# Kernel optimization log

Measured on AMD Instinct MI355X. Metric: run time of the kernel, lower is better.

The kernel has to match this reference:

```python
import jax, jax.numpy as jnp
import numpy as np

N = 100_000      # nodes
E = 3_200_000    # edges (avg degree 32)
H = 16           # hidden channels
C_IN, C_OUT = 1, 2


def setup_inputs() -> dict:
    key = jax.random.key(0)
    k1, k2, k3, k4, k5 = jax.random.split(key, 5)
    x = jax.random.normal(k1, (N, C_IN), dtype=jnp.float32)
    src = jax.random.randint(k2, (E,), 0, N, dtype=jnp.int32)
    dst = jax.random.randint(k3, (E,), 0, N, dtype=jnp.int32)
    edge_index = jnp.stack([src, dst])  # [2, E], PyG layout
    # Glorot-style init for the two linear transforms
    W1 = jax.random.normal(k4, (C_IN, H), dtype=jnp.float32) * np.sqrt(2.0 / (C_IN + H))
    b1 = jnp.zeros((H,), dtype=jnp.float32)
    W2 = jax.random.normal(k5, (H, C_OUT), dtype=jnp.float32) * np.sqrt(2.0 / (H + C_OUT))
    b2 = jnp.zeros((C_OUT,), dtype=jnp.float32)
    return {"x": x, "edge_index": edge_index, "W1": W1, "b1": b1, "W2": W2, "b2": b2}


def _gcn_conv(x, src, dst, W, b):
    """GCNConv: out = D^{-1/2} (A+I) D^{-1/2} X W + b.
    src/dst already include self-loops. x: [N, Cin], W: [Cin, Cout]."""
    deg = jax.ops.segment_sum(jnp.ones_like(dst, dtype=x.dtype), dst, num_segments=N)
    dinv = jnp.where(deg > 0, jax.lax.rsqrt(jnp.maximum(deg, 1.0)), 0.0)
    norm = dinv[src] * dinv[dst]                       # [E+N]
    h = x @ W                                          # transform first (Cin small)
    msg = norm[:, None] * h[src]                       # [E+N, Cout]
    out = jax.ops.segment_sum(msg, dst, num_segments=N)
    return out + b


def reference(x, edge_index, W1, b1, W2, b2):
    loops = jnp.arange(N, dtype=edge_index.dtype)
    src = jnp.concatenate([edge_index[0], loops])      # add self-loops
    dst = jnp.concatenate([edge_index[1], loops])
    h = _gcn_conv(x, src, dst, W1, b1)
    h = jax.nn.relu(h)
    out = _gcn_conv(h, src, dst, W2, b2)
    return out
```

## Files before the change

### kernel.cpp

```cpp
#include <hip/hip_runtime.h>

#define NN 100000
#define NE 3200000
#define HC 16

#define BKT_BITS 7
#define BKT_NODES 128
#define NB 782
#define NB1 783
#define CHUNK_S 4096
#define NCC2 782
#define NCCP 784
#define MCAP 5120
#define EPAD ((unsigned)NN << BKT_BITS)

typedef unsigned uv4 __attribute__((ext_vector_type(4)));
typedef int      iv4 __attribute__((ext_vector_type(4)));


__global__ __launch_bounds__(256) void k_sortchunk(const int* __restrict__ src,
                                                   const int* __restrict__ dst,
                                                   unsigned short* __restrict__ Hoff,
                                                   unsigned* __restrict__ binned) {
    __shared__ unsigned h[NB1];
    __shared__ unsigned sorted[CHUNK_S];
    __shared__ unsigned wsum[4];
    int tid = threadIdx.x;
    int c = blockIdx.x;
    int b0 = c * CHUNK_S;
    int e1 = min(b0 + CHUNK_S, NE);
    int cnt = e1 - b0;

    for (int j = tid; j < NB1; j += 256) h[j] = 0;
    __syncthreads();

    for (int v = b0 + tid * 4; v + 3 < e1; v += 1024) {
        iv4 d4 = *(const iv4*)(dst + v);
        atomicAdd(&h[((unsigned)d4.x) >> BKT_BITS], 1u);
        atomicAdd(&h[((unsigned)d4.y) >> BKT_BITS], 1u);
        atomicAdd(&h[((unsigned)d4.z) >> BKT_BITS], 1u);
        atomicAdd(&h[((unsigned)d4.w) >> BKT_BITS], 1u);
    }
    __syncthreads();

    int i0 = tid * 4;
    unsigned v0 = (i0 + 0 < NB1) ? h[i0 + 0] : 0;
    unsigned v1 = (i0 + 1 < NB1) ? h[i0 + 1] : 0;
    unsigned v2 = (i0 + 2 < NB1) ? h[i0 + 2] : 0;
    unsigned v3 = (i0 + 3 < NB1) ? h[i0 + 3] : 0;
    unsigned lsum = v0 + v1 + v2 + v3;
    unsigned sc = lsum;
#pragma unroll
    for (int off = 1; off < 64; off <<= 1) {
        unsigned u = __shfl_up(sc, off, 64);
        if ((tid & 63) >= off) sc += u;
    }
    int wave = tid >> 6;
    if ((tid & 63) == 63) wsum[wave] = sc;
    __syncthreads();
    unsigned wpre = 0;
    for (int w = 0; w < wave; ++w) wpre += wsum[w];
    unsigned excl = wpre + sc - lsum;
    __syncthreads();
    if (i0 + 0 < NB1) h[i0 + 0] = excl;
    if (i0 + 1 < NB1) h[i0 + 1] = excl + v0;
    if (i0 + 2 < NB1) h[i0 + 2] = excl + v0 + v1;
    if (i0 + 3 < NB1) h[i0 + 3] = excl + v0 + v1 + v2;

    unsigned short* row = Hoff + (size_t)c * NB1;
    if (i0 + 0 < NB1) row[i0 + 0] = (unsigned short)excl;
    if (i0 + 1 < NB1) row[i0 + 1] = (unsigned short)(excl + v0);
    if (i0 + 2 < NB1) row[i0 + 2] = (unsigned short)(excl + v0 + v1);
    if (i0 + 3 < NB1) row[i0 + 3] = (unsigned short)(excl + v0 + v1 + v2);
    __syncthreads();

    for (int v = b0 + tid * 4; v + 3 < e1; v += 1024) {
        iv4 d4 = *(const iv4*)(dst + v);
        iv4 s4 = *(const iv4*)(src + v);
        {   unsigned d = (unsigned)d4.x, s = (unsigned)s4.x;
            unsigned pos = atomicAdd(&h[d >> BKT_BITS], 1u);
            sorted[pos] = (s << BKT_BITS) | (d & (BKT_NODES - 1)); }
        {   unsigned d = (unsigned)d4.y, s = (unsigned)s4.y;
            unsigned pos = atomicAdd(&h[d >> BKT_BITS], 1u);
            sorted[pos] = (s << BKT_BITS) | (d & (BKT_NODES - 1)); }
        {   unsigned d = (unsigned)d4.z, s = (unsigned)s4.z;
            unsigned pos = atomicAdd(&h[d >> BKT_BITS], 1u);
            sorted[pos] = (s << BKT_BITS) | (d & (BKT_NODES - 1)); }
        {   unsigned d = (unsigned)d4.w, s = (unsigned)s4.w;
            unsigned pos = atomicAdd(&h[d >> BKT_BITS], 1u);
            sorted[pos] = (s << BKT_BITS) | (d & (BKT_NODES - 1)); }
    }
    __syncthreads();

    unsigned* out = binned + (size_t)c * CHUNK_S;
    for (int j = tid * 4; j + 3 < cnt; j += 1024)
        *(uv4*)(out + j) = *(const uv4*)(sorted + j);
}


__global__ __launch_bounds__(256) void k_transT(const unsigned short* __restrict__ Hoff,
                                                unsigned short* __restrict__ TH) {
    __shared__ unsigned short tile[32][33];
    int tx = threadIdx.x & 31;
    int ty0 = (threadIdx.x >> 5) * 4;
    int c0 = blockIdx.x * 32;
    int b0 = blockIdx.y * 32;
#pragma unroll
    for (int k = 0; k < 4; ++k) {
        int c = c0 + ty0 + k, b = b0 + tx;
        tile[ty0 + k][tx] = (c < NCC2 && b < NB1) ? Hoff[(size_t)c * NB1 + b] : (unsigned short)0;
    }
    __syncthreads();
#pragma unroll
    for (int k = 0; k < 4; ++k) {
        int b = b0 + ty0 + k, c = c0 + tx;
        if (b < NB1 && c < NCC2) TH[(size_t)b * NCCP + c] = tile[tx][ty0 + k];
    }
}


__global__ __launch_bounds__(64) void k_totals(const unsigned short* __restrict__ TH,
                                               unsigned* __restrict__ totals) {
    int b = blockIdx.x;
    int lane = threadIdx.x;
    const unsigned short* r0 = TH + (size_t)b * NCCP;
    const unsigned short* r1 = r0 + NCCP;
    unsigned s = 0;
    for (int c = lane; c < NCC2; c += 64) s += (unsigned)r1[c] - (unsigned)r0[c];
#pragma unroll
    for (int off = 32; off >= 1; off >>= 1) s += __shfl_xor(s, off, 64);
    if (lane == 0) totals[b] = s;
}

__global__ __launch_bounds__(1024) void k_base2(const unsigned* __restrict__ totals,
                                                unsigned* __restrict__ gbase) {
    __shared__ unsigned s[1024];
    int t = threadIdx.x;
    unsigned v = (t < NB) ? ((totals[t] + 15u) & ~15u) : 0;
    s[t] = v;
    __syncthreads();
    for (int off = 1; off < 1024; off <<= 1) {
        unsigned u = (t >= off) ? s[t - off] : 0;
        __syncthreads();
        s[t] += u;
        __syncthreads();
    }
    if (t < NB) gbase[t] = s[t] - v;
}


__global__ __launch_bounds__(256) void k_merge_deg(const unsigned* __restrict__ binned,
                                                   const unsigned short* __restrict__ TH,
                                                   const unsigned* __restrict__ gbase,
                                                   const float* __restrict__ x,
                                                   unsigned* __restrict__ merged,
                                                   unsigned short* __restrict__ cofsg,
                                                   float* __restrict__ dinv,
                                                   float* __restrict__ p) {
    __shared__ unsigned short th0s[NCC2];
    __shared__ unsigned short lens[NCC2];
    __shared__ unsigned S[NB1];
    __shared__ unsigned wsum[4];
    __shared__ unsigned cnt[BKT_NODES];
    __shared__ unsigned stage[MCAP];
    __shared__ unsigned short cof[BKT_NODES + 2];
    __shared__ unsigned wsA;
    int tid = threadIdx.x, b = blockIdx.x;

    const unsigned short* r0 = TH + (size_t)b * NCCP;
    const unsigned short* r1 = r0 + NCCP;
    for (int c = tid; c < NCC2; c += 256) {
        unsigned a = r0[c];
        th0s[c] = (unsigned short)a;
        lens[c] = (unsigned short)((unsigned)r1[c] - a);
    }
    if (tid < BKT_NODES) cnt[tid] = 0;
    __syncthreads();

    int i0 = tid * 4;
    unsigned v0 = (i0 + 0 < NCC2) ? (unsigned)lens[i0 + 0] : 0;
    unsigned v1 = (i0 + 1 < NCC2) ? (unsigned)lens[i0 + 1] : 0;
    unsigned v2 = (i0 + 2 < NCC2) ? (unsigned)lens[i0 + 2] : 0;
    unsigned v3 = (i0 + 3 < NCC2) ? (unsigned)lens[i0 + 3] : 0;
    unsigned lsum = v0 + v1 + v2 + v3;
    unsigned sc = lsum;
#pragma unroll
    for (int off = 1; off < 64; off <<= 1) {
        unsigned u = __shfl_up(sc, off, 64);
        if ((tid & 63) >= off) sc += u;
    }
    int wave = tid >> 6;
    if ((tid & 63) == 63) wsum[wave] = sc;
    __syncthreads();
    unsigned wpre = 0;
    for (int w = 0; w < wave; ++w) wpre += wsum[w];
    unsigned excl = wpre + sc - lsum;
    if (i0 + 0 <= NCC2) S[i0 + 0] = excl;
    if (i0 + 1 <= NCC2) S[i0 + 1] = excl + v0;
    if (i0 + 2 <= NCC2) S[i0 + 2] = excl + v0 + v1;
    if (i0 + 3 <= NCC2) S[i0 + 3] = excl + v0 + v1 + v2;
    __syncthreads();

    unsigned T = S[NCC2];
    unsigned Tr = (T + 15u) & ~15u;
    unsigned gb = gbase[b];
    if (tid < 16) {
        unsigned q = T + tid;
        if (q < Tr) stage[q] = EPAD;
    }

    for (int c = tid; c < NCC2; c += 256) {
        unsigned off = th0s[c], L = lens[c], base = S[c];
        const unsigned* seg = binned + (size_t)c * CHUNK_S + off;
        for (unsigned j = 0; j < L; ++j) {
            unsigned e = seg[j];
            atomicAdd(&cnt[e & (BKT_NODES - 1)], 1u);
            stage[base + j] = e;
        }
    }
    __syncthreads();

    for (unsigned j = tid * 4; j < Tr; j += 1024)
        *(uv4*)(merged + gb + j) = *(const uv4*)(stage + j);

    unsigned cv = (tid < BKT_NODES) ? cnt[tid] : 0u;
    unsigned csc = cv;
#pragma unroll
    for (int off = 1; off < 64; off <<= 1) {
        unsigned u = __shfl_up(csc, off, 64);
        if ((tid & 63) >= off) csc += u;
    }
    if (tid == 63) wsA = csc;
    __syncthreads();
    if (tid < BKT_NODES) {
        unsigned incl = csc + ((tid >= 64) ? wsA : 0u);
        cof[tid + 1] = (unsigned short)incl;
    }
    if (tid == 0) cof[0] = 0;
    __syncthreads();
    if (tid < BKT_NODES + 1)
        cofsg[(size_t)b * (BKT_NODES + 2) + tid] = cof[tid];

    int node = b * BKT_NODES + tid;
    if (tid < BKT_NODES) {
        if (node < NN) {
            float di = rsqrtf((float)(cnt[tid] + 1u));
            dinv[node] = di;
            p[node] = di * x[node];
        } else if (node == NN) {
            p[node] = 0.f;
        }
    }
}


__global__ __launch_bounds__(256) void k_agg1(const unsigned* __restrict__ merged,
                                              const unsigned* __restrict__ gbase,
                                              const unsigned* __restrict__ totals,
                                              const unsigned short* __restrict__ cofsg,
                                              const float* __restrict__ dinv,
                                              const float* __restrict__ p,
                                              const float* __restrict__ W1,
                                              const float* __restrict__ b1,
                                              const float* __restrict__ W2,
                                              float2* __restrict__ g) {
    __shared__ unsigned short cof[BKT_NODES + 2];
    __shared__ unsigned cur[BKT_NODES];
    __shared__ unsigned se[MCAP];
    __shared__ float part[256];
    int tid = threadIdx.x, b = blockIdx.x;
    if (tid < BKT_NODES + 1) cof[tid] = cofsg[(size_t)b * (BKT_NODES + 2) + tid];
    __syncthreads();
    if (tid < BKT_NODES) cur[tid] = cof[tid];
    __syncthreads();
    unsigned T = totals[b];
    const unsigned* m = merged + gbase[b];
    for (unsigned j = tid * 4; j < T; j += 1024) {
        uv4 e = *(const uv4*)(m + j);
        if (j + 0 < T) { unsigned w = e.x; se[atomicAdd(&cur[w & (BKT_NODES - 1)], 1u)] = w >> BKT_BITS; }
        if (j + 1 < T) { unsigned w = e.y; se[atomicAdd(&cur[w & (BKT_NODES - 1)], 1u)] = w >> BKT_BITS; }
        if (j + 2 < T) { unsigned w = e.z; se[atomicAdd(&cur[w & (BKT_NODES - 1)], 1u)] = w >> BKT_BITS; }
        if (j + 3 < T) { unsigned w = e.w; se[atomicAdd(&cur[w & (BKT_NODES - 1)], 1u)] = w >> BKT_BITS; }
    }
    __syncthreads();

    int nl = tid >> 1, half = tid & 1;
    unsigned o0 = cof[nl], o1 = cof[nl + 1];
    unsigned len = o1 - o0, mid = o0 + ((len + 1) >> 1);
    unsigned s = half ? mid : o0;
    unsigned e = half ? o1 : mid;
    float sum = 0.f;
    unsigned i = s;
    for (; i + 3 < e; i += 4) {
        unsigned a0 = se[i], a1 = se[i + 1], a2 = se[i + 2], a3 = se[i + 3];
        float x0 = p[a0], x1 = p[a1], x2 = p[a2], x3 = p[a3];
        sum += (x0 + x1) + (x2 + x3);
    }
    for (; i < e; ++i) sum += p[se[i]];
    part[tid] = sum;
    __syncthreads();

    if (!half) {
        int node = b * BKT_NODES + nl;
        if (node < NN) {
            float di = dinv[node];
            float sf = di * (part[tid] + part[tid + 1] + p[node]);
            float g0 = 0.f, g1 = 0.f;
#pragma unroll
            for (int c = 0; c < HC; ++c) {
                float h = fmaxf(fmaf(sf, W1[c], b1[c]), 0.f);
                g0 = fmaf(h, W2[2 * c], g0);
                g1 = fmaf(h, W2[2 * c + 1], g1);
            }
            g[node] = make_float2(di * g0, di * g1);
        }
    }
}


__global__ __launch_bounds__(256) void k_agg2(const unsigned* __restrict__ merged,
                                              const unsigned* __restrict__ gbase,
                                              const unsigned* __restrict__ totals,
                                              const unsigned short* __restrict__ cofsg,
                                              const float* __restrict__ dinv,
                                              const float2* __restrict__ g,
                                              const float* __restrict__ b2,
                                              float2* __restrict__ out) {
    __shared__ unsigned short cof[BKT_NODES + 2];
    __shared__ unsigned cur[BKT_NODES];
    __shared__ unsigned se[MCAP];
    __shared__ float2 part[256];
    int tid = threadIdx.x, b = blockIdx.x;
    if (tid < BKT_NODES + 1) cof[tid] = cofsg[(size_t)b * (BKT_NODES + 2) + tid];
    __syncthreads();
    if (tid < BKT_NODES) cur[tid] = cof[tid];
    __syncthreads();
    unsigned T = totals[b];
    const unsigned* m = merged + gbase[b];
    for (unsigned j = tid * 4; j < T; j += 1024) {
        uv4 e = *(const uv4*)(m + j);
        if (j + 0 < T) { unsigned w = e.x; se[atomicAdd(&cur[w & (BKT_NODES - 1)], 1u)] = w >> BKT_BITS; }
        if (j + 1 < T) { unsigned w = e.y; se[atomicAdd(&cur[w & (BKT_NODES - 1)], 1u)] = w >> BKT_BITS; }
        if (j + 2 < T) { unsigned w = e.z; se[atomicAdd(&cur[w & (BKT_NODES - 1)], 1u)] = w >> BKT_BITS; }
        if (j + 3 < T) { unsigned w = e.w; se[atomicAdd(&cur[w & (BKT_NODES - 1)], 1u)] = w >> BKT_BITS; }
    }
    __syncthreads();

    int nl = tid >> 1, half = tid & 1;
    unsigned o0 = cof[nl], o1 = cof[nl + 1];
    unsigned len = o1 - o0, mid = o0 + ((len + 1) >> 1);
    unsigned s = half ? mid : o0;
    unsigned e = half ? o1 : mid;
    float sx = 0.f, sy = 0.f;
    unsigned i = s;
    for (; i + 3 < e; i += 4) {
        unsigned a0 = se[i], a1 = se[i + 1], a2 = se[i + 2], a3 = se[i + 3];
        float2 v0 = g[a0], v1 = g[a1], v2 = g[a2], v3 = g[a3];
        sx += (v0.x + v1.x) + (v2.x + v3.x);
        sy += (v0.y + v1.y) + (v2.y + v3.y);
    }
    for (; i < e; ++i) { float2 v = g[se[i]]; sx += v.x; sy += v.y; }
    part[tid] = make_float2(sx, sy);
    __syncthreads();

    if (!half) {
        int node = b * BKT_NODES + nl;
        if (node < NN) {
            float di = dinv[node];
            float2 me = g[node];
            float ax = part[tid].x + part[tid + 1].x + me.x;
            float ay = part[tid].y + part[tid + 1].y + me.y;
            out[node] = make_float2(fmaf(di, ax, b2[0]), fmaf(di, ay, b2[1]));
        }
    }
}


__global__ __launch_bounds__(256) void f_deg(const int* __restrict__ dst,
                                             unsigned int* __restrict__ deg, int E) {
    int i = blockIdx.x * blockDim.x + threadIdx.x;
    if (i < E) atomicAdd(&deg[dst[i]], 1u);
}
__global__ __launch_bounds__(256) void f_node1(const float* __restrict__ x,
                                               const unsigned int* __restrict__ deg,
                                               float* __restrict__ dinv, float* __restrict__ p,
                                               float* __restrict__ t, int N) {
    int i = blockIdx.x * blockDim.x + threadIdx.x;
    if (i < N) {
        float di = rsqrtf((float)(deg[i] + 1u));
        dinv[i] = di; float pi = di * x[i]; p[i] = pi; t[i] = pi;
    }
}
__global__ __launch_bounds__(256) void f_scatter1(const int* __restrict__ src,
                                                  const int* __restrict__ dst,
                                                  const float* __restrict__ p,
                                                  float* __restrict__ t, int E) {
    int i = blockIdx.x * blockDim.x + threadIdx.x;
    if (i < E) atomicAdd(&t[dst[i]], p[src[i]]);
}
__global__ __launch_bounds__(256) void f_node2(const float* __restrict__ dinv,
                                               const float* __restrict__ t,
                                               const float* __restrict__ W1,
                                               const float* __restrict__ b1,
                                               const float* __restrict__ W2,
                                               float2* __restrict__ g,
                                               float2* __restrict__ acc, int N) {
    int i = blockIdx.x * blockDim.x + threadIdx.x;
    if (i < N) {
        float di = dinv[i]; float s = di * t[i];
        float g0 = 0.f, g1 = 0.f;
#pragma unroll
        for (int c = 0; c < HC; ++c) {
            float h = fmaxf(fmaf(s, W1[c], b1[c]), 0.f);
            g0 = fmaf(h, W2[2 * c], g0); g1 = fmaf(h, W2[2 * c + 1], g1);
        }
        float2 gv = make_float2(di * g0, di * g1);
        g[i] = gv; acc[i] = gv;
    }
}
__global__ __launch_bounds__(256) void f_scatter2(const int* __restrict__ src,
                                                  const int* __restrict__ dst,
                                                  const float2* __restrict__ g,
                                                  float* __restrict__ acc, int E) {
    int i = blockIdx.x * blockDim.x + threadIdx.x;
    if (i < E) {
        int s = src[i], d = dst[i];
        float2 gv = g[s];
        atomicAdd(&acc[2 * d], gv.x);
        atomicAdd(&acc[2 * d + 1], gv.y);
    }
}
__global__ __launch_bounds__(256) void f_out(const float* __restrict__ dinv,
                                             const float* __restrict__ b2,
                                             float* __restrict__ out, int N) {
    int i = blockIdx.x * blockDim.x + threadIdx.x;
    if (i < N) {
        float di = dinv[i];
        out[2 * i]     = fmaf(di, out[2 * i],     b2[0]);
        out[2 * i + 1] = fmaf(di, out[2 * i + 1], b2[1]);
    }
}

extern "C" void kernel_launch(void* const* d_in, const int* in_sizes, int n_in,
                              void* d_out, int out_size, void* d_ws, size_t ws_size,
                              hipStream_t stream) {
    const float* x  = (const float*)d_in[0];
    const int* ei   = (const int*)d_in[1];
    const int* src  = ei;
    const int* dst  = ei + NE;
    const float* W1 = (const float*)d_in[2];
    const float* b1 = (const float*)d_in[3];
    const float* W2 = (const float*)d_in[4];
    const float* b2 = (const float*)d_in[5];

    const int BT = 256;
    const int gridE = (NE + BT - 1) / BT;
    const int gridN = (NN + BT - 1) / BT;

    size_t need = 0;
    auto carve = [&](size_t bytes) { size_t o = need; need += (bytes + 255) & ~(size_t)255; return o; };
    size_t o_Hoff = carve((size_t)NCC2 * NB1 * 2);
    size_t o_TH   = carve((size_t)NB1 * NCCP * 2);
    size_t o_tot  = carve((size_t)NB * 4);
    size_t o_gb   = carve((size_t)(NB + 1) * 4);
    size_t o_cofs = carve((size_t)NB * (BKT_NODES + 2) * 2);
    size_t o_dinv = carve((size_t)NN * 4);
    size_t o_p    = carve((size_t)(NN + 1) * 4);
    size_t o_g    = carve((size_t)(NN + 1) * 8);
    size_t o_bin  = carve((size_t)NCC2 * CHUNK_S * 4);
    size_t o_mrg  = carve((size_t)(NE + 16 * NB + 64) * 4);

    if (ws_size >= need) {
        char* ws = (char*)d_ws;
        unsigned short* Hoff = (unsigned short*)(ws + o_Hoff);
        unsigned short* TH   = (unsigned short*)(ws + o_TH);
        unsigned* totals = (unsigned*)(ws + o_tot);
        unsigned* gbase  = (unsigned*)(ws + o_gb);
        unsigned short* cofs = (unsigned short*)(ws + o_cofs);
        float*    dinv   = (float*)(ws + o_dinv);
        float*    p      = (float*)(ws + o_p);
        float2*   g      = (float2*)(ws + o_g);
        unsigned* binned = (unsigned*)(ws + o_bin);
        unsigned* merged = (unsigned*)(ws + o_mrg);

        k_sortchunk<<<NCC2, 256, 0, stream>>>(src, dst, Hoff, binned);
        k_transT   <<<dim3(25, 25), 256, 0, stream>>>(Hoff, TH);
        k_totals   <<<NB, 64, 0, stream>>>(TH, totals);
        k_base2    <<<1, 1024, 0, stream>>>(totals, gbase);
        k_merge_deg<<<NB, 256, 0, stream>>>(binned, TH, gbase, x, merged, cofs, dinv, p);
        k_agg1     <<<NB, 256, 0, stream>>>(merged, gbase, totals, cofs, dinv, p, W1, b1, W2, g);
        k_agg2     <<<NB, 256, 0, stream>>>(merged, gbase, totals, cofs, dinv, g, b2, (float2*)d_out);
    } else {
        float* out = (float*)d_out;
        char* ws = (char*)d_ws;
        unsigned int* deg = (unsigned int*)ws;
        float* dinv = (float*)(ws + 1 * sizeof(float) * NN);
        float* p    = (float*)(ws + 2 * sizeof(float) * NN);
        float* t    = (float*)(ws + 3 * sizeof(float) * NN);
        float2* g   = (float2*)(ws + 4 * sizeof(float) * NN);

        hipMemsetAsync(deg, 0, NN * sizeof(unsigned int), stream);
        f_deg<<<gridE, BT, 0, stream>>>(dst, deg, NE);
        f_node1<<<gridN, BT, 0, stream>>>(x, deg, dinv, p, t, NN);
        f_scatter1<<<gridE, BT, 0, stream>>>(src, dst, p, t, NE);
        f_node2<<<gridN, BT, 0, stream>>>(dinv, t, W1, b1, W2, g, (float2*)out, NN);
        f_scatter2<<<gridE, BT, 0, stream>>>(src, dst, g, out, NE);
        f_out<<<gridN, BT, 0, stream>>>(dinv, b2, out, NN);
    }
}
```

Measured before the change: 159.7 us.

## Finalize per-node sorted edge list once in merge kernel, aggregators read from global

The per-node counting-sort scatter into a sorted source list now happens once in k_merge_deg, which writes the node-ordered source indices to global memory. k_agg1 and k_agg2 no longer rebuild that sorted list in LDS with atomics; they read neighbour indices directly from global. This removes a duplicated LDS scatter pass and its syncs from both aggregation kernels. In exchange, the merge kernel uses more shared memory (an extra 20KB buffer), which may lower occupancy, and the aggregators' index reads now go to global memory instead of LDS.

```diff
diff --git a/kernel.cpp b/kernel.cpp
--- a/kernel.cpp
+++ b/kernel.cpp
@@ -12,7 +12,6 @@
 #define NCC2 782
 #define NCCP 784
 #define MCAP 5120
-#define EPAD ((unsigned)NN << BKT_BITS)
 
 typedef unsigned uv4 __attribute__((ext_vector_type(4)));
 typedef int      iv4 __attribute__((ext_vector_type(4)));
@@ -153,7 +152,7 @@
                                                    const unsigned short* __restrict__ TH,
                                                    const unsigned* __restrict__ gbase,
                                                    const float* __restrict__ x,
-                                                   unsigned* __restrict__ merged,
+                                                   unsigned* __restrict__ se,
                                                    unsigned short* __restrict__ cofsg,
                                                    float* __restrict__ dinv,
                                                    float* __restrict__ p) {
@@ -162,7 +161,9 @@
     __shared__ unsigned S[NB1];
     __shared__ unsigned wsum[4];
     __shared__ unsigned cnt[BKT_NODES];
+    __shared__ unsigned cur[BKT_NODES];
     __shared__ unsigned stage[MCAP];
+    __shared__ unsigned se_lds[MCAP];
     __shared__ unsigned short cof[BKT_NODES + 2];
     __shared__ unsigned wsA;
     int tid = threadIdx.x, b = blockIdx.x;
@@ -204,10 +205,6 @@
     unsigned T = S[NCC2];
     unsigned Tr = (T + 15u) & ~15u;
     unsigned gb = gbase[b];
-    if (tid < 16) {
-        unsigned q = T + tid;
-        if (q < Tr) stage[q] = EPAD;
-    }
 
     for (int c = tid; c < NCC2; c += 256) {
         unsigned off = th0s[c], L = lens[c], base = S[c];
@@ -220,9 +217,6 @@
     }
     __syncthreads();
 
-    for (unsigned j = tid * 4; j < Tr; j += 1024)
-        *(uv4*)(merged + gb + j) = *(const uv4*)(stage + j);
-
     unsigned cv = (tid < BKT_NODES) ? cnt[tid] : 0u;
     unsigned csc = cv;
 #pragma unroll
@@ -235,28 +229,39 @@
     if (tid < BKT_NODES) {
         unsigned incl = csc + ((tid >= 64) ? wsA : 0u);
         cof[tid + 1] = (unsigned short)incl;
+        cur[tid] = incl - cv;
     }
     if (tid == 0) cof[0] = 0;
     __syncthreads();
+
+    for (unsigned j = tid; j < T; j += 256) {
+        unsigned w = stage[j];
+        unsigned pos = atomicAdd(&cur[w & (BKT_NODES - 1)], 1u);
+        se_lds[pos] = w >> BKT_BITS;
+    }
+    if (tid < 16) {
+        unsigned q = T + tid;
+        if (q < Tr) se_lds[q] = 0;
+    }
+    __syncthreads();
+
+    for (unsigned j = tid * 4; j < Tr; j += 1024)
+        *(uv4*)(se + gb + j) = *(const uv4*)(se_lds + j);
+
     if (tid < BKT_NODES + 1)
         cofsg[(size_t)b * (BKT_NODES + 2) + tid] = cof[tid];
 
     int node = b * BKT_NODES + tid;
-    if (tid < BKT_NODES) {
-        if (node < NN) {
-            float di = rsqrtf((float)(cnt[tid] + 1u));
-            dinv[node] = di;
-            p[node] = di * x[node];
-        } else if (node == NN) {
-            p[node] = 0.f;
-        }
-    }
-}
-
-
-__global__ __launch_bounds__(256) void k_agg1(const unsigned* __restrict__ merged,
+    if (tid < BKT_NODES && node < NN) {
+        float di = rsqrtf((float)(cnt[tid] + 1u));
+        dinv[node] = di;
+        p[node] = di * x[node];
+    }
+}
+
+
+__global__ __launch_bounds__(256) void k_agg1(const unsigned* __restrict__ se,
                                               const unsigned* __restrict__ gbase,
-                                              const unsigned* __restrict__ totals,
                                               const unsigned short* __restrict__ cofsg,
                                               const float* __restrict__ dinv,
                                               const float* __restrict__ p,
@@ -265,24 +270,11 @@
                                               const float* __restrict__ W2,
                                               float2* __restrict__ g) {
     __shared__ unsigned short cof[BKT_NODES + 2];
-    __shared__ unsigned cur[BKT_NODES];
-    __shared__ unsigned se[MCAP];
     __shared__ float part[256];
     int tid = threadIdx.x, b = blockIdx.x;
     if (tid < BKT_NODES + 1) cof[tid] = cofsg[(size_t)b * (BKT_NODES + 2) + tid];
     __syncthreads();
-    if (tid < BKT_NODES) cur[tid] = cof[tid];
-    __syncthreads();
-    unsigned T = totals[b];
-    const unsigned* m = merged + gbase[b];
-    for (unsigned j = tid * 4; j < T; j += 1024) {
-        uv4 e = *(const uv4*)(m + j);
-        if (j + 0 < T) { unsigned w = e.x; se[atomicAdd(&cur[w & (BKT_NODES - 1)], 1u)] = w >> BKT_BITS; }
-        if (j + 1 < T) { unsigned w = e.y; se[atomicAdd(&cur[w & (BKT_NODES - 1)], 1u)] = w >> BKT_BITS; }
-        if (j + 2 < T) { unsigned w = e.z; se[atomicAdd(&cur[w & (BKT_NODES - 1)], 1u)] = w >> BKT_BITS; }
-        if (j + 3 < T) { unsigned w = e.w; se[atomicAdd(&cur[w & (BKT_NODES - 1)], 1u)] = w >> BKT_BITS; }
-    }
-    __syncthreads();
+    const unsigned* m = se + gbase[b];
 
     int nl = tid >> 1, half = tid & 1;
     unsigned o0 = cof[nl], o1 = cof[nl + 1];
@@ -292,11 +284,11 @@
     float sum = 0.f;
     unsigned i = s;
     for (; i + 3 < e; i += 4) {
-        unsigned a0 = se[i], a1 = se[i + 1], a2 = se[i + 2], a3 = se[i + 3];
+        unsigned a0 = m[i], a1 = m[i + 1], a2 = m[i + 2], a3 = m[i + 3];
         float x0 = p[a0], x1 = p[a1], x2 = p[a2], x3 = p[a3];
         sum += (x0 + x1) + (x2 + x3);
     }
-    for (; i < e; ++i) sum += p[se[i]];
+    for (; i < e; ++i) sum += p[m[i]];
     part[tid] = sum;
     __syncthreads();
 
@@ -318,33 +310,19 @@
 }
 
 
-__global__ __launch_bounds__(256) void k_agg2(const unsigned* __restrict__ merged,
+__global__ __launch_bounds__(256) void k_agg2(const unsigned* __restrict__ se,
                                               const unsigned* __restrict__ gbase,
-                                              const unsigned* __restrict__ totals,
                                               const unsigned short* __restrict__ cofsg,
                                               const float* __restrict__ dinv,
                                               const float2* __restrict__ g,
                                               const float* __restrict__ b2,
                                               float2* __restrict__ out) {
     __shared__ unsigned short cof[BKT_NODES + 2];
-    __shared__ unsigned cur[BKT_NODES];
-    __shared__ unsigned se[MCAP];
     __shared__ float2 part[256];
     int tid = threadIdx.x, b = blockIdx.x;
     if (tid < BKT_NODES + 1) cof[tid] = cofsg[(size_t)b * (BKT_NODES + 2) + tid];
     __syncthreads();
-    if (tid < BKT_NODES) cur[tid] = cof[tid];
-    __syncthreads();
-    unsigned T = totals[b];
-    const unsigned* m = merged + gbase[b];
-    for (unsigned j = tid * 4; j < T; j += 1024) {
-        uv4 e = *(const uv4*)(m + j);
-        if (j + 0 < T) { unsigned w = e.x; se[atomicAdd(&cur[w & (BKT_NODES - 1)], 1u)] = w >> BKT_BITS; }
-        if (j + 1 < T) { unsigned w = e.y; se[atomicAdd(&cur[w & (BKT_NODES - 1)], 1u)] = w >> BKT_BITS; }
-        if (j + 2 < T) { unsigned w = e.z; se[atomicAdd(&cur[w & (BKT_NODES - 1)], 1u)] = w >> BKT_BITS; }
-        if (j + 3 < T) { unsigned w = e.w; se[atomicAdd(&cur[w & (BKT_NODES - 1)], 1u)] = w >> BKT_BITS; }
-    }
-    __syncthreads();
+    const unsigned* m = se + gbase[b];
 
     int nl = tid >> 1, half = tid & 1;
     unsigned o0 = cof[nl], o1 = cof[nl + 1];
@@ -354,12 +332,12 @@
     float sx = 0.f, sy = 0.f;
     unsigned i = s;
     for (; i + 3 < e; i += 4) {
-        unsigned a0 = se[i], a1 = se[i + 1], a2 = se[i + 2], a3 = se[i + 3];
+        unsigned a0 = m[i], a1 = m[i + 1], a2 = m[i + 2], a3 = m[i + 3];
         float2 v0 = g[a0], v1 = g[a1], v2 = g[a2], v3 = g[a3];
         sx += (v0.x + v1.x) + (v2.x + v3.x);
         sy += (v0.y + v1.y) + (v2.y + v3.y);
     }
-    for (; i < e; ++i) { float2 v = g[se[i]]; sx += v.x; sy += v.y; }
+    for (; i < e; ++i) { float2 v = g[m[i]]; sx += v.x; sy += v.y; }
     part[tid] = make_float2(sx, sy);
     __syncthreads();
 
@@ -468,7 +446,7 @@
     size_t o_p    = carve((size_t)(NN + 1) * 4);
     size_t o_g    = carve((size_t)(NN + 1) * 8);
     size_t o_bin  = carve((size_t)NCC2 * CHUNK_S * 4);
-    size_t o_mrg  = carve((size_t)(NE + 16 * NB + 64) * 4);
+    size_t o_se   = carve((size_t)(NE + 16 * NB + 64) * 4);
 
     if (ws_size >= need) {
         char* ws = (char*)d_ws;
@@ -481,15 +459,15 @@
         float*    p      = (float*)(ws + o_p);
         float2*   g      = (float2*)(ws + o_g);
         unsigned* binned = (unsigned*)(ws + o_bin);
-        unsigned* merged = (unsigned*)(ws + o_mrg);
+        unsigned* se     = (unsigned*)(ws + o_se);
 
         k_sortchunk<<<NCC2, 256, 0, stream>>>(src, dst, Hoff, binned);
         k_transT   <<<dim3(25, 25), 256, 0, stream>>>(Hoff, TH);
         k_totals   <<<NB, 64, 0, stream>>>(TH, totals);
         k_base2    <<<1, 1024, 0, stream>>>(totals, gbase);
-        k_merge_deg<<<NB, 256, 0, stream>>>(binned, TH, gbase, x, merged, cofs, dinv, p);
-        k_agg1     <<<NB, 256, 0, stream>>>(merged, gbase, totals, cofs, dinv, p, W1, b1, W2, g);
-        k_agg2     <<<NB, 256, 0, stream>>>(merged, gbase, totals, cofs, dinv, g, b2, (float2*)d_out);
+        k_merge_deg<<<NB, 256, 0, stream>>>(binned, TH, gbase, x, se, cofs, dinv, p);
+        k_agg1     <<<NB, 256, 0, stream>>>(se, gbase, cofs, dinv, p, W1, b1, W2, g);
+        k_agg2     <<<NB, 256, 0, stream>>>(se, gbase, cofs, dinv, g, b2, (float2*)d_out);
     } else {
         float* out = (float*)d_out;
         char* ws = (char*)d_ws;
```

New measurement: 177.0 us. 10.8% more time.
